# Kernel optimization log

Hardware: AMD Instinct MI355X
Metric: run time of the kernel (lower is better)

## Reference

```python
import jax, jax.numpy as jnp
import numpy as np

EMBED = 768
HEADS = 12
DEPTH = 12
FEAT = 2048


def _ln(x, w, b, eps=1e-6):
    m = x.mean(-1, keepdims=True)
    v = ((x - m) ** 2).mean(-1, keepdims=True)
    return (x - m) * jax.lax.rsqrt(v + eps) * w + b


def _var_attn(x, mbias, Wqkv, bqkv, Wp, bp, h, f):
    # x: (B, N, D) with N = 1 + f*n ; mbias: (B, N) additive mask (0 or -100)
    B, N, D = x.shape
    d = D // h
    n = (N - 1) // f
    scale = d ** -0.5
    qkv = x @ Wqkv.T + bqkv
    q, k, v = jnp.split(qkv, 3, axis=-1)
    hd = lambda t: t.reshape(B, N, h, d).transpose(0, 2, 1, 3)  # (B,h,N,d)
    q = hd(q) * scale
    k = hd(k)
    v = hd(v)
    # cls token attends to everything
    cls_sim = jnp.einsum('bhd,bhjd->bhj', q[:, :, 0], k) + mbias[:, None, :]
    cls_out = jnp.einsum('bhj,bhjd->bhd', jax.nn.softmax(cls_sim, axis=-1), v)[:, :, None, :]
    # spatial tokens attend within their frame plus the cls token
    q_ = q[:, :, 1:].reshape(B, h, f, n, d)
    k_ = jnp.concatenate([jnp.broadcast_to(k[:, :, None, 0:1, :], (B, h, f, 1, d)),
                          k[:, :, 1:].reshape(B, h, f, n, d)], axis=3)
    v_ = jnp.concatenate([jnp.broadcast_to(v[:, :, None, 0:1, :], (B, h, f, 1, d)),
                          v[:, :, 1:].reshape(B, h, f, n, d)], axis=3)
    mcat = jnp.concatenate([jnp.broadcast_to(mbias[:, 0][:, None, None], (B, f, 1)),
                            mbias[:, 1:].reshape(B, f, n)], axis=2)  # (B,f,n+1)
    sim = jnp.einsum('bhfid,bhfjd->bhfij', q_, k_) + mcat[:, None, :, None, :]
    out = jnp.einsum('bhfij,bhfjd->bhfid', jax.nn.softmax(sim, axis=-1), v_)
    out = out.reshape(B, h, f * n, d)
    out = jnp.concatenate([cls_out, out], axis=2).transpose(0, 2, 1, 3).reshape(B, N, D)
    return out @ Wp.T + bp


def setup_inputs() -> dict:
    key = jax.random.key(0)
    ks = jax.random.split(key, 12)
    B, F, L = 256, 4, 20
    std = 0.02
    p = {}
    p['x'] = jax.random.normal(ks[0], (B, F, L, 2054), dtype=jnp.float32)
    p['x_mask'] = jax.random.randint(ks[1], (B, F, L), 0, 2, dtype=jnp.int32)
    p['obj_W'] = (jax.random.normal(ks[2], (EMBED, FEAT)) * std).astype(jnp.float32)
    p['obj_b'] = jnp.zeros((EMBED,), jnp.float32)
    p['pos_W'] = (jax.random.normal(ks[3], (EMBED, 6)) * std).astype(jnp.float32)
    p['pos_b'] = jnp.zeros((EMBED,), jnp.float32)
    p['cls_token'] = (jax.random.normal(ks[4], (1, 1, EMBED)) * std).astype(jnp.float32)
    p['cls_pos'] = (jax.random.normal(ks[5], (1, L + 1, EMBED)) * std).astype(jnp.float32)
    p['temporal_embed'] = jnp.zeros((1, F, EMBED), jnp.float32)
    p['ln1_w'] = jnp.ones((DEPTH, EMBED), jnp.float32)
    p['ln1_b'] = jnp.zeros((DEPTH, EMBED), jnp.float32)
    p['ln2_w'] = jnp.ones((DEPTH, EMBED), jnp.float32)
    p['ln2_b'] = jnp.zeros((DEPTH, EMBED), jnp.float32)
    p['qkv_W'] = (jax.random.normal(ks[6], (DEPTH, 3 * EMBED, EMBED)) * std).astype(jnp.float32)
    p['qkv_b'] = jnp.zeros((DEPTH, 3 * EMBED), jnp.float32)
    p['ap_W'] = (jax.random.normal(ks[7], (DEPTH, EMBED, EMBED)) * std).astype(jnp.float32)
    p['ap_b'] = jnp.zeros((DEPTH, EMBED), jnp.float32)
    p['fc1_W'] = (jax.random.normal(ks[8], (DEPTH, 4 * EMBED, EMBED)) * std).astype(jnp.float32)
    p['fc1_b'] = jnp.zeros((DEPTH, 4 * EMBED), jnp.float32)
    p['fc2_W'] = (jax.random.normal(ks[9], (DEPTH, EMBED, 4 * EMBED)) * std).astype(jnp.float32)
    p['fc2_b'] = jnp.zeros((DEPTH, EMBED), jnp.float32)
    p['proj_W'] = (jax.random.normal(ks[10], (256, EMBED)) * std).astype(jnp.float32)
    return p


def reference(x, x_mask, obj_W, obj_b, pos_W, pos_b, cls_token, cls_pos, temporal_embed,
              ln1_w, ln1_b, ln2_w, ln2_b, qkv_W, qkv_b, ap_W, ap_b,
              fc1_W, fc1_b, fc2_W, fc2_b, proj_W):
    B, F, L, _ = x.shape
    tok = x[..., :FEAT] @ obj_W.T + obj_b + (x[..., FEAT:] @ pos_W.T + pos_b)
    tok = tok.reshape(B, F * L, EMBED)
    m = x_mask.reshape(B, F * L).astype(tok.dtype)
    tok = jnp.concatenate([jnp.broadcast_to(cls_token, (B, 1, EMBED)), tok], axis=1)
    m = jnp.concatenate([jnp.ones((B, 1), tok.dtype), m], axis=1)
    mbias = (m - 1.0) * 100.0  # 0 for valid, -100 for padded
    pos_total = jnp.concatenate([cls_pos[:, 0:1, :], jnp.repeat(temporal_embed, L, axis=1)], axis=1)
    tok = tok + pos_total

    def body(xc, p):
        l1w, l1b, qW, qb, aW, ab, l2w, l2b, f1W, f1b, f2W, f2b = p
        a = _var_attn(_ln(xc, l1w, l1b), mbias, qW, qb, aW, ab, HEADS, F)
        xr = xc + a
        xc = xr + (jax.nn.gelu(_ln(xr, l2w, l2b) @ f1W.T + f1b, approximate=False) @ f2W.T + f2b)
        return xc, None

    tok, _ = jax.lax.scan(body, tok, (ln1_w, ln1_b, qkv_W, qkv_b, ap_W, ap_b,
                                      ln2_w, ln2_b, fc1_W, fc1_b, fc2_W, fc2_b))
    return tok @ proj_W.T, mbias
```

## Files before the change

### kernel.cpp

```cpp
#include <hip/hip_runtime.h>

typedef __bf16 bf16;
typedef __bf16 bf16x8 __attribute__((ext_vector_type(8)));
typedef float f32x4 __attribute__((ext_vector_type(4)));

#define EMBED 768
#define HEADS 12
#define DEPTH 12
#define B_ 256
#define F_ 4
#define L_ 20
#define NTOK 81
#define ROWS (B_ * NTOK)
#define SROWS (B_ * F_ * L_)

#define GLOAD16(g, l)                                                              \
    __builtin_amdgcn_global_load_lds((const __attribute__((address_space(1))) void*)(g), \
                                     (__attribute__((address_space(3))) void*)(l), 16, 0, 0)

__device__ __forceinline__ float fast_gelu(float v) {
    float x = v * 0.70710678118654752f;
    float ax = fabsf(x);
    float t = __fdividef(1.f, fmaf(0.3275911f, ax, 1.f));
    float p = ((((1.061405429f * t - 1.453152027f) * t + 1.421413741f) * t -
                0.284496736f) * t + 0.254829592f) * t;
    float e = __expf(-ax * ax);
    float erfv = copysignf(1.f - p * e, x);
    return 0.5f * v * (1.f + erfv);
}

__global__ __launch_bounds__(256) void repack_kernel(const float* __restrict__ x,
                                                     bf16* __restrict__ xr) {
    int row = blockIdx.x;
    const float* src = x + (size_t)row * 2054;
    bf16* dst = xr + (size_t)row * 2048;
    int t = threadIdx.x;
    int e0 = t * 8;
    bf16 tmp[8];
#pragma unroll
    for (int i = 0; i < 4; ++i) {
        float2 v = *(const float2*)&src[e0 + 2 * i];
        tmp[2 * i] = (bf16)v.x;
        tmp[2 * i + 1] = (bf16)v.y;
    }
    *(uint4*)&dst[e0] = *(const uint4*)tmp;
}

__global__ __launch_bounds__(256) void w2bf_kernel(const float* __restrict__ src,
                                                   bf16* __restrict__ dst) {
    size_t i = ((size_t)blockIdx.x * 256 + threadIdx.x) * 8;
    float4 a = *(const float4*)&src[i];
    float4 b = *(const float4*)&src[i + 4];
    bf16 t[8] = {(bf16)a.x, (bf16)a.y, (bf16)a.z, (bf16)a.w,
                 (bf16)b.x, (bf16)b.y, (bf16)b.z, (bf16)b.w};
    *(uint4*)&dst[i] = *(const uint4*)t;
}

template <int FUSE, bool ROWMAP, typename CT>
__global__ __launch_bounds__(512, 2) void gemm_256(const bf16* __restrict__ A, int lda,
                                                   const bf16* __restrict__ W,
                                                   const float* __restrict__ bias,
                                                   const bf16* __restrict__ R,
                                                   CT* __restrict__ C, int N, int K) {
    __shared__ __align__(16) char smem[131072];

    const int tid = threadIdx.x;
    const int lane = tid & 63;
    const int wv = tid >> 6;
    const int wm = (wv >> 2) * 128;
    const int wn = (wv & 3) * 64;
    const int lr = lane & 15;
    const int lq = lane >> 4;

    const int GX = gridDim.x;
    const int nwg = GX * gridDim.y;
    const int flat = blockIdx.y * GX + blockIdx.x;
    const int xcd = flat & 7, pos = flat >> 3;
    const int qc = nwg >> 3, rc = nwg & 7;
    const int wg = (xcd < rc ? xcd * (qc + 1) : rc * (qc + 1) + (xcd - rc) * qc) + pos;
    const int n0 = (wg % GX) * 256;
    const int m0 = (wg / GX) * 256;

    const int srow = lane >> 3;
    const int scol = 8 * ((lane & 7) ^ srow);
    const bf16* aP[4];
    const bf16* wP[4];
#pragma unroll
    for (int i = 0; i < 4; ++i) {
        aP[i] = A + (size_t)(m0 + wv * 32 + i * 8 + srow) * lda + scol;
        wP[i] = W + (size_t)(n0 + wv * 32 + i * 8 + srow) * K + scol;
    }

    f32x4 acc[8][4];
#pragma unroll
    for (int i = 0; i < 8; ++i)
#pragma unroll
        for (int j = 0; j < 4; ++j) acc[i][j] = (f32x4){0.f, 0.f, 0.f, 0.f};

    const int swz = (lr & 7) << 4;
    const int co0 = (((0 << 6) | (lq << 4)) ^ swz) >> 1;
    const int co1 = (((1 << 6) | (lq << 4)) ^ swz) >> 1;

    const int nk = K >> 6;

#pragma unroll
    for (int i = 0; i < 4; ++i) {
        GLOAD16(aP[i], smem + (wv * 4 + i) * 1024);
        GLOAD16(wP[i], smem + 32768 + (wv * 4 + i) * 1024);
    }
    asm volatile("s_waitcnt vmcnt(0)" ::: "memory");
    __builtin_amdgcn_sched_barrier(0);
    __builtin_amdgcn_s_barrier();

    int c = 0;
    for (int t = 0; t < nk; ++t) {
        if (t + 1 < nk) {
            const int koff = (t + 1) << 6;
            char* dst = smem + (c ^ 1) * 65536 + (wv * 4) * 1024;
#pragma unroll
            for (int i = 0; i < 4; ++i) {
                GLOAD16(aP[i] + koff, dst + i * 1024);
                GLOAD16(wP[i] + koff, dst + 32768 + i * 1024);
            }
            __builtin_amdgcn_sched_barrier(0);
        }
        {
            const bf16* As_ = (const bf16*)(smem + c * 65536);
            const bf16* Bs_ = (const bf16*)(smem + c * 65536 + 32768);
            bf16x8 bw0[4], bw1[4];
#pragma unroll
            for (int ni = 0; ni < 4; ++ni) {
                const int br = (wn + ni * 16 + lr) * 64;
                bw0[ni] = *(const bf16x8*)&Bs_[br + co0];
                bw1[ni] = *(const bf16x8*)&Bs_[br + co1];
            }
            __builtin_amdgcn_s_setprio(1);
#pragma unroll
            for (int mi = 0; mi < 8; ++mi) {
                const int ar = (wm + mi * 16 + lr) * 64;
                bf16x8 a0 = *(const bf16x8*)&As_[ar + co0];
                bf16x8 a1 = *(const bf16x8*)&As_[ar + co1];
#pragma unroll
                for (int ni = 0; ni < 4; ++ni) {
                    acc[mi][ni] =
                        __builtin_amdgcn_mfma_f32_16x16x32_bf16(a0, bw0[ni], acc[mi][ni], 0, 0, 0);
                    acc[mi][ni] =
                        __builtin_amdgcn_mfma_f32_16x16x32_bf16(a1, bw1[ni], acc[mi][ni], 0, 0, 0);
                }
            }
            __builtin_amdgcn_s_setprio(0);
        }
        if (t + 1 < nk) {
            asm volatile("s_waitcnt vmcnt(0)" ::: "memory");
            __builtin_amdgcn_sched_barrier(0);
            __builtin_amdgcn_s_barrier();
        }
        c ^= 1;
    }

    __builtin_amdgcn_s_barrier();
    float* patch = (float*)(smem + wv * 4352);
    float bv4[4];
#pragma unroll
    for (int ni = 0; ni < 4; ++ni) bv4[ni] = bias ? bias[n0 + wn + ni * 16 + lr] : 0.f;
    const int rr = lane >> 3;
    const int c8 = (lane & 7) * 8;
#pragma unroll
    for (int mi = 0; mi < 8; ++mi) {
#pragma unroll
        for (int ni = 0; ni < 4; ++ni)
#pragma unroll
            for (int r = 0; r < 4; ++r)
                patch[(lq * 4 + r) * 68 + ni * 16 + lr] = acc[mi][ni][r] + bv4[ni];
#pragma unroll
        for (int hf = 0; hf < 2; ++hf) {
            int row = rr + hf * 8;
            float v[8];
            *(float4*)&v[0] = *(const float4*)&patch[row * 68 + c8];
            *(float4*)&v[4] = *(const float4*)&patch[row * 68 + c8 + 4];
            int grow = m0 + wm + mi * 16 + row;
            int gcol = n0 + wn + c8;
            if (FUSE == 1) {
#pragma unroll
                for (int q = 0; q < 8; ++q) v[q] = fast_gelu(v[q]);
            }
            if (FUSE == 2) {
                bf16x8 rv = *(const bf16x8*)&R[(size_t)grow * N + gcol];
#pragma unroll
                for (int q = 0; q < 8; ++q) v[q] += (float)rv[q];
            }
            int orow = grow;
            if (ROWMAP) orow = grow + grow / 80 + 1;
            if constexpr (sizeof(CT) == 2) {
                bf16 ob[8];
#pragma unroll
                for (int q = 0; q < 8; ++q) ob[q] = (bf16)v[q];
                *(uint4*)&C[(size_t)orow * N + gcol] = *(const uint4*)ob;
            } else {
                *(float4*)&C[(size_t)orow * N + gcol] = *(const float4*)&v[0];
                *(float4*)&C[(size_t)orow * N + gcol + 4] = *(const float4*)&v[4];
            }
        }
    }
}

template <int FUSE, bool ROWMAP, typename CT>
__global__ __launch_bounds__(256) void gemm_bb(const bf16* __restrict__ A, int lda,
                                               const bf16* __restrict__ W,
                                               const float* __restrict__ bias,
                                               const bf16* __restrict__ R,
                                               CT* __restrict__ C, int N, int K) {
    __shared__ __align__(16) char smem[32768];

    const int tid = threadIdx.x;
    const int lane = tid & 63;
    const int wv = tid >> 6;
    const int wm = (wv & 1) * 64;
    const int wn = (wv >> 1) * 64;
    const int lr = lane & 15;
    const int lq = lane >> 4;

    const int GX = gridDim.x;
    const int nwg = GX * gridDim.y;
    const int flat = blockIdx.y * GX + blockIdx.x;
    const int xcd = flat & 7, pos = flat >> 3;
    const int qc = nwg >> 3, rc = nwg & 7;
    const int wg = (xcd < rc ? xcd * (qc + 1) : rc * (qc + 1) + (xcd - rc) * qc) + pos;
    const int n0 = (wg % GX) * 128;
    const int m0 = (wg / GX) * 128;

    const int srow = lane >> 3;
    const int scol = 8 * ((lane & 7) ^ srow);
    const bf16* aB = A + (size_t)(m0 + srow) * lda + scol;
    const bf16* wB = W + (size_t)(n0 + srow) * K + scol;

    bf16* As = (bf16*)smem;
    bf16* Ws = (bf16*)(smem + 16384);

    f32x4 acc[4][4];
#pragma unroll
    for (int i = 0; i < 4; ++i)
#pragma unroll
        for (int j = 0; j < 4; ++j) acc[i][j] = (f32x4){0.f, 0.f, 0.f, 0.f};

    const int swz = (lr & 7) << 4;

    for (int k0 = 0; k0 < K; k0 += 64) {
#pragma unroll
        for (int i = 0; i < 4; ++i) {
            const int ch = wv * 4 + i;
            GLOAD16(aB + (size_t)(ch * 8) * lda + k0, smem + ch * 1024);
            GLOAD16(wB + (size_t)(ch * 8) * K + k0, smem + 16384 + ch * 1024);
        }
        __syncthreads();
#pragma unroll
        for (int kk = 0; kk < 2; ++kk) {
            const int co = (((kk << 6) | (lq << 4)) ^ swz) >> 1;
            bf16x8 af[4], bw[4];
#pragma unroll
            for (int t = 0; t < 4; ++t) {
                af[t] = *(const bf16x8*)&As[(wm + t * 16 + lr) * 64 + co];
                bw[t] = *(const bf16x8*)&Ws[(wn + t * 16 + lr) * 64 + co];
            }
#pragma unroll
            for (int mi = 0; mi < 4; ++mi)
#pragma unroll
                for (int ni = 0; ni < 4; ++ni)
                    acc[mi][ni] = __builtin_amdgcn_mfma_f32_16x16x32_bf16(af[mi], bw[ni],
                                                                          acc[mi][ni], 0, 0, 0);
        }
        __syncthreads();
    }

    float* patch = (float*)(smem + wv * 4352);
    float bv4[4];
#pragma unroll
    for (int ni = 0; ni < 4; ++ni) bv4[ni] = bias ? bias[n0 + wn + ni * 16 + lr] : 0.f;
    const int rr = lane >> 3;
    const int c8 = (lane & 7) * 8;
#pragma unroll
    for (int mi = 0; mi < 4; ++mi) {
#pragma unroll
        for (int ni = 0; ni < 4; ++ni)
#pragma unroll
            for (int r = 0; r < 4; ++r)
                patch[(lq * 4 + r) * 68 + ni * 16 + lr] = acc[mi][ni][r] + bv4[ni];
#pragma unroll
        for (int hf = 0; hf < 2; ++hf) {
            int row = rr + hf * 8;
            float v[8];
            *(float4*)&v[0] = *(const float4*)&patch[row * 68 + c8];
            *(float4*)&v[4] = *(const float4*)&patch[row * 68 + c8 + 4];
            int grow = m0 + wm + mi * 16 + row;
            int gcol = n0 + wn + c8;
            if (FUSE == 1) {
#pragma unroll
                for (int q = 0; q < 8; ++q) v[q] = fast_gelu(v[q]);
            }
            if (FUSE == 2) {
                bf16x8 rv = *(const bf16x8*)&R[(size_t)grow * N + gcol];
#pragma unroll
                for (int q = 0; q < 8; ++q) v[q] += (float)rv[q];
            }
            int orow = grow;
            if (ROWMAP) orow = grow + grow / 80 + 1;
            if constexpr (sizeof(CT) == 2) {
                bf16 ob[8];
#pragma unroll
                for (int q = 0; q < 8; ++q) ob[q] = (bf16)v[q];
                *(uint4*)&C[(size_t)orow * N + gcol] = *(const uint4*)ob;
            } else {
                *(float4*)&C[(size_t)orow * N + gcol] = *(const float4*)&v[0];
                *(float4*)&C[(size_t)orow * N + gcol + 4] = *(const float4*)&v[4];
            }
        }
    }
}

template <int FUSE, bool ROWMAP, typename CT>
__global__ __launch_bounds__(256) void gemm_bt(const bf16* __restrict__ A, int lda,
                                               const float* __restrict__ W,
                                               const float* __restrict__ bias,
                                               const bf16* __restrict__ R,
                                               CT* __restrict__ C, int N, int K) {
    __shared__ __align__(16) bf16 As[128][32];
    __shared__ __align__(16) bf16 Ws[128][32];

    const int tid = threadIdx.x;
    const int lane = tid & 63;
    const int wv = tid >> 6;
    const int wm = (wv & 1) * 64;
    const int wn = (wv >> 1) * 64;
    const int lr = lane & 15;
    const int lq = lane >> 4;
    const int m0 = blockIdx.x * 128;
    const int n0 = blockIdx.y * 128;

    f32x4 acc[4][4];
#pragma unroll
    for (int i = 0; i < 4; ++i)
#pragma unroll
        for (int j = 0; j < 4; ++j) acc[i][j] = (f32x4){0.f, 0.f, 0.f, 0.f};

    for (int k0 = 0; k0 < K; k0 += 32) {
#pragma unroll
        for (int i = 0; i < 2; ++i) {
            int c = tid + 256 * i;
            int row = c >> 2;
            int kc = (c & 3) * 8;
            *(uint4*)&As[row][kc] = *(const uint4*)&A[(size_t)(m0 + row) * lda + k0 + kc];
        }
#pragma unroll
        for (int i = 0; i < 4; ++i) {
            int c = tid + 256 * i;
            int row = c >> 3;
            int kc = (c & 7) * 4;
            float4 v = *(const float4*)&W[(size_t)(n0 + row) * K + k0 + kc];
            bf16 wb[4] = {(bf16)v.x, (bf16)v.y, (bf16)v.z, (bf16)v.w};
            *(uint2*)&Ws[row][kc] = *(const uint2*)wb;
        }
        __syncthreads();
        bf16x8 af[4], bf_[4];
#pragma unroll
        for (int t = 0; t < 4; ++t) {
            af[t] = *(const bf16x8*)&As[wm + t * 16 + lr][lq * 8];
            bf_[t] = *(const bf16x8*)&Ws[wn + t * 16 + lr][lq * 8];
        }
#pragma unroll
        for (int mi = 0; mi < 4; ++mi)
#pragma unroll
            for (int ni = 0; ni < 4; ++ni)
                acc[mi][ni] = __builtin_amdgcn_mfma_f32_16x16x32_bf16(af[mi], bf_[ni],
                                                                      acc[mi][ni], 0, 0, 0);
        __syncthreads();
    }

#pragma unroll
    for (int mi = 0; mi < 4; ++mi) {
#pragma unroll
        for (int ni = 0; ni < 4; ++ni) {
            int gcol = n0 + wn + ni * 16 + lr;
            float bv = bias ? bias[gcol] : 0.f;
#pragma unroll
            for (int r = 0; r < 4; ++r) {
                int grow = m0 + wm + mi * 16 + lq * 4 + r;
                float v = acc[mi][ni][r] + bv;
                if (FUSE == 1) v = fast_gelu(v);
                if (FUSE == 2) v += (float)R[(size_t)grow * N + gcol];
                int orow = grow;
                if (ROWMAP) orow = grow + grow / 80 + 1;
                C[(size_t)orow * N + gcol] = (CT)v;
            }
        }
    }
}

__global__ __launch_bounds__(256) void embed_finish(const float* __restrict__ x,
                                                    const float* __restrict__ posW,
                                                    const float* __restrict__ posb,
                                                    const float* __restrict__ temb,
                                                    bf16* __restrict__ tok) {
    int r = blockIdx.x;
    int fr = (r % 80) / 20;
    int orow = r + r / 80 + 1;
    __shared__ float pf[6];
    if (threadIdx.x < 6) pf[threadIdx.x] = x[(size_t)r * 2054 + 2048 + threadIdx.x];
    __syncthreads();
    int t = threadIdx.x;
#pragma unroll
    for (int i = 0; i < 3; ++i) {
        int c = t + 256 * i;
        float v = posb[c] + temb[fr * EMBED + c];
#pragma unroll
        for (int j = 0; j < 6; ++j) v += pf[j] * posW[c * 6 + j];
        size_t idx = (size_t)orow * EMBED + c;
        tok[idx] = (bf16)((float)tok[idx] + v);
    }
}

__global__ __launch_bounds__(256) void cls_mbias_kernel(const float* __restrict__ cls_tok,
                                                        const float* __restrict__ cls_pos,
                                                        const int* __restrict__ xmask,
                                                        bf16* __restrict__ tok,
                                                        float* __restrict__ mbias,
                                                        float* __restrict__ out1) {
    int b = blockIdx.x;
    int t = threadIdx.x;
#pragma unroll
    for (int i = 0; i < 3; ++i) {
        int c = t + 256 * i;
        tok[(size_t)(b * NTOK) * EMBED + c] = (bf16)(cls_tok[c] + cls_pos[c]);
    }
    if (t < NTOK) {
        float mv = (t == 0) ? 0.f : ((float)xmask[b * 80 + t - 1] - 1.f) * 100.f;
        mbias[b * NTOK + t] = mv;
        out1[b * NTOK + t] = mv;
    }
}

__global__ __launch_bounds__(256) void ln_kernel(const bf16* __restrict__ X,
                                                 const float* __restrict__ w,
                                                 const float* __restrict__ b,
                                                 bf16* __restrict__ Y) {
    int half = threadIdx.x >> 7;
    int row = blockIdx.x * 2 + half;
    int tt = threadIdx.x & 127;
    float xv[8];
    float s = 0.f, ss = 0.f;
    if (tt < 96) {
        bf16x8 v8 = *(const bf16x8*)&X[(size_t)row * EMBED + tt * 8];
#pragma unroll
        for (int i = 0; i < 8; ++i) {
            float v = (float)v8[i];
            xv[i] = v;
            s += v;
            ss += v * v;
        }
    }
#pragma unroll
    for (int off = 32; off; off >>= 1) {
        s += __shfl_down(s, off);
        ss += __shfl_down(ss, off);
    }
    __shared__ float ws_s[4], ws_q[4];
    int wv = threadIdx.x >> 6, lane = threadIdx.x & 63;
    if (lane == 0) { ws_s[wv] = s; ws_q[wv] = ss; }
    __syncthreads();
    s = ws_s[half * 2] + ws_s[half * 2 + 1];
    ss = ws_q[half * 2] + ws_q[half * 2 + 1];
    float mean = s * (1.f / 768.f);
    float var = ss * (1.f / 768.f) - mean * mean;
    float inv = rsqrtf(fmaxf(var, 0.f) + 1e-6f);
    if (tt < 96) {
        float4 w0 = *(const float4*)&w[tt * 8];
        float4 w1 = *(const float4*)&w[tt * 8 + 4];
        float4 b0 = *(const float4*)&b[tt * 8];
        float4 b1 = *(const float4*)&b[tt * 8 + 4];
        float wr[8] = {w0.x, w0.y, w0.z, w0.w, w1.x, w1.y, w1.z, w1.w};
        float br[8] = {b0.x, b0.y, b0.z, b0.w, b1.x, b1.y, b1.z, b1.w};
        bf16 ob[8];
#pragma unroll
        for (int i = 0; i < 8; ++i) ob[i] = (bf16)((xv[i] - mean) * inv * wr[i] + br[i]);
        *(uint4*)&Y[(size_t)row * EMBED + tt * 8] = *(const uint4*)ob;
    }
}

__global__ __launch_bounds__(256) void attn_kernel(const bf16* __restrict__ qkv,
                                                   const float* __restrict__ mbias,
                                                   bf16* __restrict__ aout) {
    int bh = blockIdx.x;
    int b = bh / HEADS, h = bh % HEADS;
    __shared__ __align__(16) float Qf[NTOK][68];
    __shared__ __align__(16) float Kf[NTOK][68];
    __shared__ __align__(16) bf16 Vs[NTOK][72];
    __shared__ float S[80][22];
    __shared__ float Sc[96];
    __shared__ float MB[NTOK];
    const size_t base = (size_t)(b * NTOK) * 2304 + h * 64;
    int t = threadIdx.x;

    for (int ch = t; ch < NTOK * 8; ch += 256) {
        int r = ch >> 3, c8 = (ch & 7) * 8;
        size_t o = base + (size_t)r * 2304 + c8;
        bf16x8 qv = *(const bf16x8*)&qkv[o];
        bf16x8 kv = *(const bf16x8*)&qkv[o + 768];
        *(uint4*)&Vs[r][c8] = *(const uint4*)&qkv[o + 1536];
        float4 q0 = {(float)qv[0], (float)qv[1], (float)qv[2], (float)qv[3]};
        float4 q1 = {(float)qv[4], (float)qv[5], (float)qv[6], (float)qv[7]};
        float4 k0 = {(float)kv[0], (float)kv[1], (float)kv[2], (float)kv[3]};
        float4 k1 = {(float)kv[4], (float)kv[5], (float)kv[6], (float)kv[7]};
        *(float4*)&Qf[r][c8] = q0;
        *(float4*)&Qf[r][c8 + 4] = q1;
        *(float4*)&Kf[r][c8] = k0;
        *(float4*)&Kf[r][c8 + 4] = k1;
    }
    if (t < NTOK) MB[t] = mbias[b * NTOK + t];
    __syncthreads();

    {
        int qt = (t < 240) ? 1 + t / 3 : 0;
        float fq[64];
#pragma unroll
        for (int i = 0; i < 16; ++i) {
            float4 v = *(const float4*)&Qf[qt][i * 4];
            fq[4 * i] = v.x; fq[4 * i + 1] = v.y; fq[4 * i + 2] = v.z; fq[4 * i + 3] = v.w;
        }
        if (t < 240) {
            int qi = t / 3, fb = (qi / 20) * 20, kst = t - qi * 3;
            for (int kj = kst; kj < 21; kj += 3) {
                int kt = (kj == 0) ? 0 : fb + kj;
                float acc = 0.f;
#pragma unroll
                for (int i = 0; i < 16; ++i) {
                    float4 kv = *(const float4*)&Kf[kt][i * 4];
                    acc += fq[4 * i] * kv.x + fq[4 * i + 1] * kv.y +
                           fq[4 * i + 2] * kv.z + fq[4 * i + 3] * kv.w;
                }
                S[qi][kj] = acc * 0.125f + MB[kt];
            }
        } else {
            for (int kt = t - 240; kt < NTOK; kt += 16) {
                float acc = 0.f;
#pragma unroll
                for (int i = 0; i < 16; ++i) {
                    float4 kv = *(const float4*)&Kf[kt][i * 4];
                    acc += fq[4 * i] * kv.x + fq[4 * i + 1] * kv.y +
                           fq[4 * i + 2] * kv.z + fq[4 * i + 3] * kv.w;
                }
                Sc[kt] = acc * 0.125f + MB[kt];
            }
        }
    }
    __syncthreads();

    if (t < 80) {
        float mx = -1e30f;
        for (int j = 0; j < 21; ++j) mx = fmaxf(mx, S[t][j]);
        float sum = 0.f;
        for (int j = 0; j < 21; ++j) { float e = __expf(S[t][j] - mx); S[t][j] = e; sum += e; }
        float rs = 1.f / sum;
        for (int j = 0; j < 21; ++j) S[t][j] *= rs;
    } else if (t == 80) {
        float mx = -1e30f;
        for (int j = 0; j < NTOK; ++j) mx = fmaxf(mx, Sc[j]);
        float sum = 0.f;
        for (int j = 0; j < NTOK; ++j) { float e = __expf(Sc[j] - mx); Sc[j] = e; sum += e; }
        float rs = 1.f / sum;
        for (int j = 0; j < NTOK; ++j) Sc[j] *= rs;
    }
    __syncthreads();

    for (int idx = t; idx < NTOK * 8; idx += 256) {
        int r = idx >> 3, c8 = (idx & 7) * 8;
        float acc[8];
#pragma unroll
        for (int q = 0; q < 8; ++q) acc[q] = 0.f;
        if (r == 0) {
            for (int j = 0; j < NTOK; ++j) {
                float w = Sc[j];
                bf16x8 vv = *(const bf16x8*)&Vs[j][c8];
#pragma unroll
                for (int q = 0; q < 8; ++q) acc[q] += w * (float)vv[q];
            }
        } else {
            int qi = r - 1, fb = (qi / 20) * 20;
            {
                float w = S[qi][0];
                bf16x8 vv = *(const bf16x8*)&Vs[0][c8];
#pragma unroll
                for (int q = 0; q < 8; ++q) acc[q] += w * (float)vv[q];
            }
            for (int j = 1; j < 21; ++j) {
                float w = S[qi][j];
                bf16x8 vv = *(const bf16x8*)&Vs[fb + j][c8];
#pragma unroll
                for (int q = 0; q < 8; ++q) acc[q] += w * (float)vv[q];
            }
        }
        bf16 ob[8];
#pragma unroll
        for (int q = 0; q < 8; ++q) ob[q] = (bf16)acc[q];
        *(uint4*)&aout[(size_t)(b * NTOK + r) * EMBED + h * 64 + c8] = *(const uint4*)ob;
    }
}

extern "C" void kernel_launch(void* const* d_in, const int* in_sizes, int n_in,
                              void* d_out, int out_size, void* d_ws, size_t ws_size,
                              hipStream_t stream) {
    const float* x = (const float*)d_in[0];
    const int* xmask = (const int*)d_in[1];
    const float* objW = (const float*)d_in[2];
    const float* objb = (const float*)d_in[3];
    const float* posW = (const float*)d_in[4];
    const float* posb = (const float*)d_in[5];
    const float* clsT = (const float*)d_in[6];
    const float* clsP = (const float*)d_in[7];
    const float* temb = (const float*)d_in[8];
    const float* ln1w = (const float*)d_in[9];
    const float* ln1b = (const float*)d_in[10];
    const float* ln2w = (const float*)d_in[11];
    const float* ln2b = (const float*)d_in[12];
    const float* qkvW = (const float*)d_in[13];
    const float* qkvb = (const float*)d_in[14];
    const float* apW = (const float*)d_in[15];
    const float* apb = (const float*)d_in[16];
    const float* f1W = (const float*)d_in[17];
    const float* f1b = (const float*)d_in[18];
    const float* f2W = (const float*)d_in[19];
    const float* f2b = (const float*)d_in[20];
    const float* projW = (const float*)d_in[21];

    char* ws = (char*)d_ws;
    bf16* tok = (bf16*)(ws);
    bf16* s1 = (bf16*)(ws + (size_t)(32 << 20));
    float* mb = (float*)(ws + (size_t)(64 << 20));
    bf16* big = (bf16*)(ws + (size_t)(65 << 20));
    float* out0 = (float*)d_out;
    float* out1 = out0 + (size_t)ROWS * 256;

    const size_t WOFF = (size_t)192 << 20;
    const size_t E_OBJ = (size_t)768 * 2048;
    const size_t E_QKV = (size_t)DEPTH * 2304 * 768;
    const size_t E_AP = (size_t)DEPTH * 768 * 768;
    const size_t E_FC = (size_t)DEPTH * 3072 * 768;
    const size_t E_PROJ = (size_t)256 * 768;
    const size_t WTOT = (E_OBJ + E_QKV + E_AP + 2 * E_FC + E_PROJ) * 2;
    const bool bigws = ws_size >= WOFF + WTOT;

    if (bigws) {
        bf16* objW16 = (bf16*)(ws + WOFF);
        bf16* qkvW16 = objW16 + E_OBJ;
        bf16* apW16 = qkvW16 + E_QKV;
        bf16* fc1W16 = apW16 + E_AP;
        bf16* fc2W16 = fc1W16 + E_FC;
        bf16* projW16 = fc2W16 + E_FC;

        w2bf_kernel<<<(int)(E_OBJ / 2048), 256, 0, stream>>>(objW, objW16);
        w2bf_kernel<<<(int)(E_QKV / 2048), 256, 0, stream>>>(qkvW, qkvW16);
        w2bf_kernel<<<(int)(E_AP / 2048), 256, 0, stream>>>(apW, apW16);
        w2bf_kernel<<<(int)(E_FC / 2048), 256, 0, stream>>>(f1W, fc1W16);
        w2bf_kernel<<<(int)(E_FC / 2048), 256, 0, stream>>>(f2W, fc2W16);
        w2bf_kernel<<<(int)(E_PROJ / 2048), 256, 0, stream>>>(projW, projW16);

        repack_kernel<<<SROWS, 256, 0, stream>>>(x, big);
        gemm_256<0, true, bf16><<<dim3(EMBED / 256, SROWS / 256), 512, 0, stream>>>(
            big, 2048, objW16, objb, nullptr, tok, EMBED, 2048);
        embed_finish<<<SROWS, 256, 0, stream>>>(x, posW, posb, temb, tok);
        cls_mbias_kernel<<<B_, 256, 0, stream>>>(clsT, clsP, xmask, tok, mb, out1);

        for (int l = 0; l < DEPTH; ++l) {
            ln_kernel<<<ROWS / 2, 256, 0, stream>>>(tok, ln1w + l * EMBED, ln1b + l * EMBED, s1);
            gemm_256<0, false, bf16><<<dim3(2304 / 256, ROWS / 256), 512, 0, stream>>>(
                s1, EMBED, qkvW16 + (size_t)l * 2304 * 768, qkvb + l * 2304, nullptr, big,
                2304, EMBED);
            attn_kernel<<<B_ * HEADS, 256, 0, stream>>>(big, mb, s1);
            gemm_256<2, false, bf16><<<dim3(EMBED / 256, ROWS / 256), 512, 0, stream>>>(
                s1, EMBED, apW16 + (size_t)l * 768 * 768, apb + l * EMBED, tok, tok, EMBED,
                EMBED);
            ln_kernel<<<ROWS / 2, 256, 0, stream>>>(tok, ln2w + l * EMBED, ln2b + l * EMBED, s1);
            gemm_256<1, false, bf16><<<dim3(3072 / 256, ROWS / 256), 512, 0, stream>>>(
                s1, EMBED, fc1W16 + (size_t)l * 3072 * 768, f1b + l * 3072, nullptr, big,
                3072, EMBED);
            gemm_256<2, false, bf16><<<dim3(EMBED / 256, ROWS / 256), 512, 0, stream>>>(
                big, 3072, fc2W16 + (size_t)l * 3072 * 768, f2b + l * EMBED, tok, tok, EMBED,
                3072);
        }

        gemm_bb<0, false, float><<<dim3(256 / 128, ROWS / 128), 256, 0, stream>>>(
            tok, EMBED, projW16, nullptr, nullptr, out0, 256, EMBED);
    } else {
        repack_kernel<<<SROWS, 256, 0, stream>>>(x, big);
        gemm_bt<0, true, bf16><<<dim3(SROWS / 128, EMBED / 128), 256, 0, stream>>>(
            big, 2048, objW, objb, nullptr, tok, EMBED, 2048);
        embed_finish<<<SROWS, 256, 0, stream>>>(x, posW, posb, temb, tok);
        cls_mbias_kernel<<<B_, 256, 0, stream>>>(clsT, clsP, xmask, tok, mb, out1);

        for (int l = 0; l < DEPTH; ++l) {
            ln_kernel<<<ROWS / 2, 256, 0, stream>>>(tok, ln1w + l * EMBED, ln1b + l * EMBED, s1);
            gemm_bt<0, false, bf16><<<dim3(ROWS / 128, 2304 / 128), 256, 0, stream>>>(
                s1, EMBED, qkvW + (size_t)l * 2304 * EMBED, qkvb + l * 2304, nullptr, big,
                2304, EMBED);
            attn_kernel<<<B_ * HEADS, 256, 0, stream>>>(big, mb, s1);
            gemm_bt<2, false, bf16><<<dim3(ROWS / 128, EMBED / 128), 256, 0, stream>>>(
                s1, EMBED, apW + (size_t)l * EMBED * EMBED, apb + l * EMBED, tok, tok, EMBED,
                EMBED);
            ln_kernel<<<ROWS / 2, 256, 0, stream>>>(tok, ln2w + l * EMBED, ln2b + l * EMBED, s1);
            gemm_bt<1, false, bf16><<<dim3(ROWS / 128, 3072 / 128), 256, 0, stream>>>(
                s1, EMBED, f1W + (size_t)l * 3072 * EMBED, f1b + l * 3072, nullptr, big, 3072,
                EMBED);
            gemm_bt<2, false, bf16><<<dim3(ROWS / 128, EMBED / 128), 256, 0, stream>>>(
                big, 3072, f2W + (size_t)l * EMBED * 3072, f2b + l * EMBED, tok, tok, EMBED,
                3072);
        }

        gemm_bt<0, false, float><<<dim3(ROWS / 128, 256 / 128), 256, 0, stream>>>(
            tok, EMBED, projW, nullptr, nullptr, out0, 256, EMBED);
    }
}
```

Baseline: 6.180 ms.

## Restructure GEMM main loop into barrier-interleaved quadrant MFMA schedule

The GEMM mainloop is reorganised into a two-stage ping-pong that handles two K-tiles per iteration. Each tile's MFMA work is split into four quadrants separated by workgroup barriers, and the next A and B tile loads are issued in between quadrants so global-to-LDS traffic overlaps compute. The waits become partial (vmcnt(8)) instead of full drains. This adds more barriers per tile and assumes nk is even, which relies on K being a multiple of 128.

```diff
diff --git a/kernel.cpp b/kernel.cpp
--- a/kernel.cpp
+++ b/kernel.cpp
@@ -18,6 +18,14 @@
     __builtin_amdgcn_global_load_lds((const __attribute__((address_space(1))) void*)(g), \
                                      (__attribute__((address_space(3))) void*)(l), 16, 0, 0)
 
+#define MFMA16(a, b, c) __builtin_amdgcn_mfma_f32_16x16x32_bf16((a), (b), (c), 0, 0, 0)
+
+#define SBAR()                                   \
+    do {                                         \
+        __builtin_amdgcn_s_barrier();            \
+        __builtin_amdgcn_sched_barrier(0);       \
+    } while (0)
+
 __device__ __forceinline__ float fast_gelu(float v) {
     float x = v * 0.70710678118654752f;
     float ax = fabsf(x);
@@ -98,8 +106,8 @@
         for (int j = 0; j < 4; ++j) acc[i][j] = (f32x4){0.f, 0.f, 0.f, 0.f};
 
     const int swz = (lr & 7) << 4;
-    const int co0 = (((0 << 6) | (lq << 4)) ^ swz) >> 1;
-    const int co1 = (((1 << 6) | (lq << 4)) ^ swz) >> 1;
+    const int co0 = ((lq << 4) ^ swz) >> 1;
+    const int co1 = ((64 | (lq << 4)) ^ swz) >> 1;
 
     const int nk = K >> 6;
 
@@ -108,57 +116,186 @@
         GLOAD16(aP[i], smem + (wv * 4 + i) * 1024);
         GLOAD16(wP[i], smem + 32768 + (wv * 4 + i) * 1024);
     }
-    asm volatile("s_waitcnt vmcnt(0)" ::: "memory");
+#pragma unroll
+    for (int i = 0; i < 4; ++i) {
+        GLOAD16(aP[i] + 64, smem + 65536 + (wv * 4 + i) * 1024);
+        GLOAD16(wP[i] + 64, smem + 65536 + 32768 + (wv * 4 + i) * 1024);
+    }
+    asm volatile("s_waitcnt vmcnt(8)" ::: "memory");
     __builtin_amdgcn_sched_barrier(0);
-    __builtin_amdgcn_s_barrier();
-
-    int c = 0;
-    for (int t = 0; t < nk; ++t) {
-        if (t + 1 < nk) {
-            const int koff = (t + 1) << 6;
-            char* dst = smem + (c ^ 1) * 65536 + (wv * 4) * 1024;
-#pragma unroll
-            for (int i = 0; i < 4; ++i) {
-                GLOAD16(aP[i] + koff, dst + i * 1024);
-                GLOAD16(wP[i] + koff, dst + 32768 + i * 1024);
-            }
-            __builtin_amdgcn_sched_barrier(0);
-        }
+    SBAR();
+
+    for (int t0 = 0; t0 < nk; t0 += 2) {
+        const bool stg = (t0 + 2 < nk);
+        const int koff = (t0 + 2) << 6;
+        bf16x8 b0[4], b1[4], a0k0[4], a0k1[4], a1k0[4], a1k1[4];
+
         {
-            const bf16* As_ = (const bf16*)(smem + c * 65536);
-            const bf16* Bs_ = (const bf16*)(smem + c * 65536 + 32768);
-            bf16x8 bw0[4], bw1[4];
+            const bf16* As_ = (const bf16*)(smem);
+            const bf16* Bs_ = (const bf16*)(smem + 32768);
 #pragma unroll
             for (int ni = 0; ni < 4; ++ni) {
                 const int br = (wn + ni * 16 + lr) * 64;
-                bw0[ni] = *(const bf16x8*)&Bs_[br + co0];
-                bw1[ni] = *(const bf16x8*)&Bs_[br + co1];
-            }
+                b0[ni] = *(const bf16x8*)&Bs_[br + co0];
+                b1[ni] = *(const bf16x8*)&Bs_[br + co1];
+            }
+#pragma unroll
+            for (int mi = 0; mi < 4; ++mi) {
+                const int ar = (wm + mi * 16 + lr) * 64;
+                a0k0[mi] = *(const bf16x8*)&As_[ar + co0];
+                a0k1[mi] = *(const bf16x8*)&As_[ar + co1];
+            }
+            SBAR();
             __builtin_amdgcn_s_setprio(1);
 #pragma unroll
-            for (int mi = 0; mi < 8; ++mi) {
+            for (int mi = 0; mi < 4; ++mi)
+#pragma unroll
+                for (int ni = 0; ni < 2; ++ni) {
+                    acc[mi][ni] = MFMA16(a0k0[mi], b0[ni], acc[mi][ni]);
+                    acc[mi][ni] = MFMA16(a0k1[mi], b1[ni], acc[mi][ni]);
+                }
+            __builtin_amdgcn_s_setprio(0);
+            __builtin_amdgcn_sched_barrier(0);
+#pragma unroll
+            for (int mi = 0; mi < 4; ++mi) {
+                const int ar = (wm + 64 + mi * 16 + lr) * 64;
+                a1k0[mi] = *(const bf16x8*)&As_[ar + co0];
+                a1k1[mi] = *(const bf16x8*)&As_[ar + co1];
+            }
+            SBAR();
+            __builtin_amdgcn_s_setprio(1);
+#pragma unroll
+            for (int mi = 0; mi < 4; ++mi)
+#pragma unroll
+                for (int ni = 2; ni < 4; ++ni) {
+                    acc[mi][ni] = MFMA16(a0k0[mi], b0[ni], acc[mi][ni]);
+                    acc[mi][ni] = MFMA16(a0k1[mi], b1[ni], acc[mi][ni]);
+                }
+            __builtin_amdgcn_s_setprio(0);
+            __builtin_amdgcn_sched_barrier(0);
+            if (stg) {
+#pragma unroll
+                for (int i = 0; i < 4; ++i)
+                    GLOAD16(aP[i] + koff, smem + (wv * 4 + i) * 1024);
+            }
+            SBAR();
+            __builtin_amdgcn_s_setprio(1);
+#pragma unroll
+            for (int mi = 0; mi < 4; ++mi)
+#pragma unroll
+                for (int ni = 0; ni < 2; ++ni) {
+                    acc[4 + mi][ni] = MFMA16(a1k0[mi], b0[ni], acc[4 + mi][ni]);
+                    acc[4 + mi][ni] = MFMA16(a1k1[mi], b1[ni], acc[4 + mi][ni]);
+                }
+            __builtin_amdgcn_s_setprio(0);
+            __builtin_amdgcn_sched_barrier(0);
+            if (stg) {
+#pragma unroll
+                for (int i = 0; i < 4; ++i)
+                    GLOAD16(wP[i] + koff, smem + 32768 + (wv * 4 + i) * 1024);
+            }
+            SBAR();
+            __builtin_amdgcn_s_setprio(1);
+#pragma unroll
+            for (int mi = 0; mi < 4; ++mi)
+#pragma unroll
+                for (int ni = 2; ni < 4; ++ni) {
+                    acc[4 + mi][ni] = MFMA16(a1k0[mi], b0[ni], acc[4 + mi][ni]);
+                    acc[4 + mi][ni] = MFMA16(a1k1[mi], b1[ni], acc[4 + mi][ni]);
+                }
+            __builtin_amdgcn_s_setprio(0);
+            if (stg) {
+                asm volatile("s_waitcnt vmcnt(8)" ::: "memory");
+            } else {
+                asm volatile("s_waitcnt vmcnt(0)" ::: "memory");
+            }
+            __builtin_amdgcn_sched_barrier(0);
+            SBAR();
+        }
+
+        {
+            const bf16* As_ = (const bf16*)(smem + 65536);
+            const bf16* Bs_ = (const bf16*)(smem + 65536 + 32768);
+#pragma unroll
+            for (int ni = 0; ni < 4; ++ni) {
+                const int br = (wn + ni * 16 + lr) * 64;
+                b0[ni] = *(const bf16x8*)&Bs_[br + co0];
+                b1[ni] = *(const bf16x8*)&Bs_[br + co1];
+            }
+#pragma unroll
+            for (int mi = 0; mi < 4; ++mi) {
                 const int ar = (wm + mi * 16 + lr) * 64;
-                bf16x8 a0 = *(const bf16x8*)&As_[ar + co0];
-                bf16x8 a1 = *(const bf16x8*)&As_[ar + co1];
-#pragma unroll
-                for (int ni = 0; ni < 4; ++ni) {
-                    acc[mi][ni] =
-                        __builtin_amdgcn_mfma_f32_16x16x32_bf16(a0, bw0[ni], acc[mi][ni], 0, 0, 0);
-                    acc[mi][ni] =
-                        __builtin_amdgcn_mfma_f32_16x16x32_bf16(a1, bw1[ni], acc[mi][ni], 0, 0, 0);
-                }
-            }
+                a0k0[mi] = *(const bf16x8*)&As_[ar + co0];
+                a0k1[mi] = *(const bf16x8*)&As_[ar + co1];
+            }
+            SBAR();
+            __builtin_amdgcn_s_setprio(1);
+#pragma unroll
+            for (int mi = 0; mi < 4; ++mi)
+#pragma unroll
+                for (int ni = 0; ni < 2; ++ni) {
+                    acc[mi][ni] = MFMA16(a0k0[mi], b0[ni], acc[mi][ni]);
+                    acc[mi][ni] = MFMA16(a0k1[mi], b1[ni], acc[mi][ni]);
+                }
             __builtin_amdgcn_s_setprio(0);
-        }
-        if (t + 1 < nk) {
-            asm volatile("s_waitcnt vmcnt(0)" ::: "memory");
             __builtin_amdgcn_sched_barrier(0);
-            __builtin_amdgcn_s_barrier();
-        }
-        c ^= 1;
-    }
-
-    __builtin_amdgcn_s_barrier();
+#pragma unroll
+            for (int mi = 0; mi < 4; ++mi) {
+                const int ar = (wm + 64 + mi * 16 + lr) * 64;
+                a1k0[mi] = *(const bf16x8*)&As_[ar + co0];
+                a1k1[mi] = *(const bf16x8*)&As_[ar + co1];
+            }
+            SBAR();
+            __builtin_amdgcn_s_setprio(1);
+#pragma unroll
+            for (int mi = 0; mi < 4; ++mi)
+#pragma unroll
+                for (int ni = 2; ni < 4; ++ni) {
+                    acc[mi][ni] = MFMA16(a0k0[mi], b0[ni], acc[mi][ni]);
+                    acc[mi][ni] = MFMA16(a0k1[mi], b1[ni], acc[mi][ni]);
+                }
+            __builtin_amdgcn_s_setprio(0);
+            __builtin_amdgcn_sched_barrier(0);
+            if (stg) {
+#pragma unroll
+                for (int i = 0; i < 4; ++i)
+                    GLOAD16(aP[i] + koff + 64, smem + 65536 + (wv * 4 + i) * 1024);
+            }
+            SBAR();
+            __builtin_amdgcn_s_setprio(1);
+#pragma unroll
+            for (int mi = 0; mi < 4; ++mi)
+#pragma unroll
+                for (int ni = 0; ni < 2; ++ni) {
+                    acc[4 + mi][ni] = MFMA16(a1k0[mi], b0[ni], acc[4 + mi][ni]);
+                    acc[4 + mi][ni] = MFMA16(a1k1[mi], b1[ni], acc[4 + mi][ni]);
+                }
+            __builtin_amdgcn_s_setprio(0);
+            __builtin_amdgcn_sched_barrier(0);
+            if (stg) {
+#pragma unroll
+                for (int i = 0; i < 4; ++i)
+                    GLOAD16(wP[i] + koff + 64, smem + 65536 + 32768 + (wv * 4 + i) * 1024);
+            }
+            SBAR();
+            __builtin_amdgcn_s_setprio(1);
+#pragma unroll
+            for (int mi = 0; mi < 4; ++mi)
+#pragma unroll
+                for (int ni = 2; ni < 4; ++ni) {
+                    acc[4 + mi][ni] = MFMA16(a1k0[mi], b0[ni], acc[4 + mi][ni]);
+                    acc[4 + mi][ni] = MFMA16(a1k1[mi], b1[ni], acc[4 + mi][ni]);
+                }
+            __builtin_amdgcn_s_setprio(0);
+            if (stg) {
+                asm volatile("s_waitcnt vmcnt(8)" ::: "memory");
+                __builtin_amdgcn_sched_barrier(0);
+                SBAR();
+            }
+        }
+    }
+
+    SBAR();
     float* patch = (float*)(smem + wv * 4352);
     float bv4[4];
 #pragma unroll
```

New measurement: 6.306 ms. 1.02x slower.
